# Optimization experiments

Hardware: AMD Instinct MI355X
Metric: run time of the kernel (lower is better)

The kernel has to match this reference:

```python
import jax, jax.numpy as jnp
import numpy as np

B, S, D, H = 2, 2048, 1024, 16
HD = D // H  # head_dim = 64
ROPE_BASE = 10000.0
INIT_STD = 0.02


def setup_inputs() -> dict:
    key = jax.random.key(0)
    k1, k2, k3 = jax.random.split(key, 3)
    x = jax.random.normal(k1, (B, S, D), dtype=jnp.float32)
    w_qkv = jax.random.normal(k2, (3 * D, D), dtype=jnp.float32) * INIT_STD
    w_out = jax.random.normal(k3, (D, D), dtype=jnp.float32) * (1.0 / np.sqrt(D))
    b_out = jnp.zeros((D,), dtype=jnp.float32)
    return {"x": x, "w_qkv": w_qkv, "w_out": w_out, "b_out": b_out}


def _rope_cos_sin(s_len, head_dim, dtype):
    theta = 1.0 / ROPE_BASE ** (jnp.arange(0, head_dim, 2, dtype=jnp.float32) / head_dim)
    freqs = jnp.outer(jnp.arange(s_len, dtype=jnp.float32), theta)  # [s, d/2]
    freqs = jnp.concatenate([freqs, freqs], axis=-1)  # [s, d]
    return jnp.cos(freqs).astype(dtype), jnp.sin(freqs).astype(dtype)


def _apply_rope(qk, cos, sin):
    # qk: [b, h, s, d]; rotate-half: (-x2, x1)
    d2 = qk.shape[-1] // 2
    x1, x2 = qk[..., :d2], qk[..., d2:]
    rot = jnp.concatenate([-x2, x1], axis=-1)
    return qk * cos + rot * sin


def reference(x, w_qkv, w_out, b_out):
    b, s, d = x.shape
    qkv = jnp.einsum('bsd,ed->bse', x, w_qkv)  # [b, s, 3D]
    qkv = qkv.reshape(b, s, 3 * H, HD).transpose(0, 2, 1, 3)  # [b, 3h, s, d]
    qk, v = qkv[:, :2 * H], qkv[:, 2 * H:]
    cos, sin = _rope_cos_sin(s, HD, x.dtype)
    qk = _apply_rope(qk, cos, sin)
    q, k = qk[:, :H], qk[:, H:]
    scale = 1.0 / np.sqrt(HD)
    scores = jnp.einsum('bhqd,bhkd->bhqk', q, k) * scale  # [b, h, s, s]
    causal = jnp.tril(jnp.ones((s, s), dtype=bool))
    scores = jnp.where(causal, scores, jnp.finfo(scores.dtype).min)
    attn = jax.nn.softmax(scores, axis=-1)
    o = jnp.einsum('bhqk,bhkd->bhqd', attn, v)  # [b, h, s, d]
    o = o.transpose(0, 2, 1, 3).reshape(b, s, d)
    return jnp.einsum('bsd,ed->bse', o, w_out) + b_out
```

## Files before the change

### kernel.cpp

```cpp
#include <hip/hip_runtime.h>
#include <hip/hip_fp16.h>
#include <math.h>

#define B_  2
#define S_  2048
#define D_  1024
#define H_  16
#define HD_ 64

typedef _Float16  f16;
typedef __attribute__((ext_vector_type(8))) _Float16 f16x8;
typedef __attribute__((ext_vector_type(4))) _Float16 f16x4;
typedef __attribute__((ext_vector_type(4))) float    f32x4;

#define LOG2E 1.4426950408889634f
#define L2_10000_DIV32 0.41524101186092029f
#define PS 72

__device__ __forceinline__ float fin(float v) { return (v == v) ? v : 0.0f; }

__device__ __forceinline__ f16x8 cvt8(const float* p) {
  float4 a = *(const float4*)p;
  float4 b = *(const float4*)(p + 4);
  f16x8 h;
  h[0] = (f16)a.x; h[1] = (f16)a.y; h[2] = (f16)a.z; h[3] = (f16)a.w;
  h[4] = (f16)b.x; h[5] = (f16)b.y; h[6] = (f16)b.z; h[7] = (f16)b.w;
  return h;
}

__global__ void __launch_bounds__(256)
k_cvt3(const float* __restrict__ wq, const float* __restrict__ wo,
       const float* __restrict__ x,
       f16* __restrict__ wqh, f16* __restrict__ woh, f16* __restrict__ xh,
       int doX)
{
  const int NWQ = 3 * D_ * D_ / 4, NWO = D_ * D_ / 4, NX = B_ * S_ * D_ / 4;
  const int n = NWQ + NWO + (doX ? NX : 0);
  for (int i = blockIdx.x * 256 + threadIdx.x; i < n; i += gridDim.x * 256) {
    const float* src; f16* dst; int j;
    if (i < NWQ)            { src = wq; dst = wqh; j = i; }
    else if (i < NWQ + NWO) { src = wo; dst = woh; j = i - NWQ; }
    else                    { src = x;  dst = xh;  j = i - NWQ - NWO; }
    float4 v = ((const float4*)src)[j];
    f16x4 h = {(f16)v.x, (f16)v.y, (f16)v.z, (f16)v.w};
    ((f16x4*)dst)[j] = h;
  }
}

template <bool XF16>
__global__ void __launch_bounds__(256)
k_qkv3(const float* __restrict__ xf, const f16* __restrict__ xh,
       const f16* __restrict__ wqh,
       f16* __restrict__ Qb, f16* __restrict__ Kb, f16* __restrict__ Vt)
{
  __shared__ __align__(16) f16 As[128 * PS];
  __shared__ __align__(16) f16 Bs[128 * PS];
  const int t = threadIdx.x;
  const int w = t >> 6;
  const int lane = t & 63;
  const int ll = lane & 15;
  const int quad = lane >> 4;
  const int wm = w >> 1, wn = w & 1;
  const int row0 = blockIdx.y * 128;
  const int col0 = blockIdx.x * 128;

  const f32x4 fz = {0.f, 0.f, 0.f, 0.f};
  f32x4 acc[4][4];
#pragma unroll
  for (int i = 0; i < 4; ++i)
#pragma unroll
    for (int j = 0; j < 4; ++j) acc[i][j] = fz;

  const int ldr = t >> 3;
  const int ldk = (t & 7) * 8;
  const float* gaf = xf  + (size_t)(row0 + ldr) * D_ + ldk;
  const f16*   gah = xh  + (size_t)(row0 + ldr) * D_ + ldk;
  const f16*   gb  = wqh + (size_t)(col0 + ldr) * D_ + ldk;

  for (int kt = 0; kt < D_; kt += 64) {
    f16x8 ra[4], rb[4];
#pragma unroll
    for (int i = 0; i < 4; ++i) {
      ra[i] = XF16 ? *(const f16x8*)(gah + (size_t)i * 32 * D_ + kt)
                   : cvt8(gaf + (size_t)i * 32 * D_ + kt);
      rb[i] = *(const f16x8*)(gb + (size_t)i * 32 * D_ + kt);
    }
    __syncthreads();
#pragma unroll
    for (int i = 0; i < 4; ++i) {
      *(f16x8*)&As[(i * 32 + ldr) * PS + ldk] = ra[i];
      *(f16x8*)&Bs[(i * 32 + ldr) * PS + ldk] = rb[i];
    }
    __syncthreads();
#pragma unroll
    for (int kk = 0; kk < 64; kk += 32) {
      f16x8 a[4], b[4];
#pragma unroll
      for (int mt = 0; mt < 4; ++mt)
        a[mt] = *(const f16x8*)&As[(wm * 64 + mt * 16 + ll) * PS + kk + quad * 8];
#pragma unroll
      for (int nt = 0; nt < 4; ++nt)
        b[nt] = *(const f16x8*)&Bs[(wn * 64 + nt * 16 + ll) * PS + kk + quad * 8];
#pragma unroll
      for (int mt = 0; mt < 4; ++mt)
#pragma unroll
        for (int nt = 0; nt < 4; ++nt)
          acc[mt][nt] = __builtin_amdgcn_mfma_f32_16x16x32_f16(
              a[mt], b[nt], acc[mt][nt], 0, 0, 0);
    }
  }

  const int h3 = (col0 >> 6) + wn;
  if (h3 < 32) {
    f16* dst = (h3 < 16) ? Qb : Kb;
    const int h = (h3 < 16) ? h3 : h3 - 16;
    const float th0 = exp2f(-(float)ll * L2_10000_DIV32);
    const float th1 = exp2f(-(float)(16 + ll) * L2_10000_DIV32);
#pragma unroll
    for (int mt = 0; mt < 4; ++mt) {
#pragma unroll
      for (int r = 0; r < 4; ++r) {
        const int row = row0 + wm * 64 + mt * 16 + quad * 4 + r;
        const int b = row >> 11;
        const int p = row & (S_ - 1);
        f16* base = dst + ((size_t)(b * H_ + h) * S_ + p) * HD_;
        const float fp = (float)p;
        float s0, c0, s1, c1;
        sincosf(fp * th0, &s0, &c0);
        sincosf(fp * th1, &s1, &c1);
        {
          float x1 = acc[mt][0][r], x2 = acc[mt][2][r];
          base[ll]      = (f16)fin(x1 * c0 - x2 * s0);
          base[ll + 32] = (f16)fin(x2 * c0 + x1 * s0);
        }
        {
          float x1 = acc[mt][1][r], x2 = acc[mt][3][r];
          base[16 + ll]      = (f16)fin(x1 * c1 - x2 * s1);
          base[16 + ll + 32] = (f16)fin(x2 * c1 + x1 * s1);
        }
      }
    }
  } else {
    const int hv = h3 - 32;
#pragma unroll
    for (int mt = 0; mt < 4; ++mt)
#pragma unroll
      for (int nt = 0; nt < 4; ++nt)
#pragma unroll
        for (int r = 0; r < 4; ++r) {
          const int row = row0 + wm * 64 + mt * 16 + quad * 4 + r;
          const int b = row >> 11;
          const int p = row & (S_ - 1);
          const int dd = nt * 16 + ll;
          Vt[((size_t)(b * H_ + hv) * HD_ + dd) * S_ + p] = (f16)fin(acc[mt][nt][r]);
        }
  }
}

__device__ __forceinline__ void softmax_tile(
    f32x4 sc[4], bool diag, int qloc, int ll, int quad,
    float& mrun, float& lrun, float& alpha, f16* Pt)
{
  if (diag) {
#pragma unroll
    for (int nt = 0; nt < 4; ++nt)
#pragma unroll
      for (int r = 0; r < 4; ++r)
        if ((nt * 16 + quad * 4 + r) > qloc) sc[nt][r] = -3.0e4f;
  }
  float pm = mrun;
#pragma unroll
  for (int nt = 0; nt < 4; ++nt)
#pragma unroll
    for (int r = 0; r < 4; ++r) pm = fmaxf(pm, sc[nt][r]);
  pm = fmaxf(pm, __shfl_xor(pm, 16));
  pm = fmaxf(pm, __shfl_xor(pm, 32));
  alpha = exp2f(mrun - pm);
  mrun = pm;
  float ps = 0.f;
#pragma unroll
  for (int nt = 0; nt < 4; ++nt) {
    f16x4 pk;
#pragma unroll
    for (int r = 0; r < 4; ++r) {
      float p = exp2f(sc[nt][r] - pm);
      ps += p;
      pk[r] = (f16)p;
    }
    *(f16x4*)&Pt[ll * PS + nt * 16 + quad * 4] = pk;
  }
  ps += __shfl_xor(ps, 16);
  ps += __shfl_xor(ps, 32);
  lrun = lrun * alpha + ps;
}

__device__ __forceinline__ void write_o(
    f32x4 acco[4], float lrun, f16* Pt, int ll, int quad, int w,
    int qt, size_t bh, f16* Ob)
{
  const float inv = 1.0f / fmaxf(lrun, 1e-30f);
#pragma unroll
  for (int dg = 0; dg < 4; ++dg) {
    f16x4 ov;
#pragma unroll
    for (int r = 0; r < 4; ++r) ov[r] = (f16)fin(acco[dg][r] * inv);
    *(f16x4*)&Pt[ll * PS + dg * 16 + quad * 4] = ov;
  }
#pragma unroll
  for (int s2 = 0; s2 < 2; ++s2) {
    f16x8 o = *(const f16x8*)&Pt[ll * PS + (quad + 4 * s2) * 8];
    const size_t row = bh * S_ + qt * 64 + w * 16 + ll;
    *(f16x8*)&Ob[row * HD_ + (quad + 4 * s2) * 8] = o;
  }
}

__global__ void __launch_bounds__(256, 3)
k_attn3(const f16* Qb, const f16* __restrict__ Kb,
        const f16* __restrict__ Vt, f16* Ob)
{
  __shared__ __align__(16) f16 Ks[2][64 * PS];
  __shared__ __align__(16) f16 Vs[2][64 * PS];
  __shared__ __align__(16) f16 Ps[4][16 * PS];

  const int t = threadIdx.x;
  const int w = t >> 6;
  const int lane = t & 63;
  const int ll = lane & 15;
  const int quad = lane >> 4;
  const int qtA = blockIdx.x;
  const int qtB = 31 - qtA;
  const int h = blockIdx.y;
  const int b = blockIdx.z;
  const size_t bh = (size_t)b * H_ + h;
  const f16* Qg = Qb + bh * S_ * HD_;
  const f16* Kg = Kb + bh * S_ * HD_;
  const f16* Vg = Vt + bh * HD_ * S_;

  f16x8 bqA[2], bqB[2];
  {
    const f16 hsc = (f16)(0.125f * LOG2E);
#pragma unroll
    for (int k2 = 0; k2 < 2; ++k2) {
      bqA[k2] = *(const f16x8*)(Qg + (size_t)(qtA * 64 + w * 16 + ll) * HD_ + k2 * 32 + quad * 8);
      bqB[k2] = *(const f16x8*)(Qg + (size_t)(qtB * 64 + w * 16 + ll) * HD_ + k2 * 32 + quad * 8);
#pragma unroll
      for (int e = 0; e < 8; ++e) { bqA[k2][e] *= hsc; bqB[k2][e] *= hsc; }
    }
  }
  {
    const int r = t >> 2;
    const int c = (t & 3) * 16;
    f16x8 a0 = *(const f16x8*)(Kg + (size_t)r * HD_ + c);
    f16x8 a1 = *(const f16x8*)(Kg + (size_t)r * HD_ + c + 8);
    f16x8 b0 = *(const f16x8*)(Vg + (size_t)r * S_ + c);
    f16x8 b1 = *(const f16x8*)(Vg + (size_t)r * S_ + c + 8);
    *(f16x8*)&Ks[0][r * PS + c]     = a0;
    *(f16x8*)&Ks[0][r * PS + c + 8] = a1;
    *(f16x8*)&Vs[0][r * PS + c]     = b0;
    *(f16x8*)&Vs[0][r * PS + c + 8] = b1;
  }
  __syncthreads();

  const f32x4 fz = {0.f, 0.f, 0.f, 0.f};
  f32x4 accoA[4], accoB[4];
#pragma unroll
  for (int i = 0; i < 4; ++i) { accoA[i] = fz; accoB[i] = fz; }
  float mA = -3.0e4f, lA = 0.f, mB = -3.0e4f, lB = 0.f;
  const int qloc = w * 16 + ll;
  f16* Pt = &Ps[w][0];

  for (int kt = 0; kt <= qtB; ++kt) {
    const int cur = kt & 1;
    const bool pre = (kt < qtB);
    const int sr = t >> 2, scc = (t & 3) * 16;
    f16x8 nk0, nk1, nv0, nv1;
    if (pre) {
      const int kn = (kt + 1) * 64;
      nk0 = *(const f16x8*)(Kg + (size_t)(kn + sr) * HD_ + scc);
      nk1 = *(const f16x8*)(Kg + (size_t)(kn + sr) * HD_ + scc + 8);
      nv0 = *(const f16x8*)(Vg + (size_t)sr * S_ + kn + scc);
      nv1 = *(const f16x8*)(Vg + (size_t)sr * S_ + kn + scc + 8);
    }
    const f16* Kc = Ks[cur];
    const f16* Vc = Vs[cur];
    const bool doA = (kt <= qtA);

    f16x8 ak[2][4];
#pragma unroll
    for (int k2 = 0; k2 < 2; ++k2)
#pragma unroll
      for (int nt = 0; nt < 4; ++nt)
        ak[k2][nt] = *(const f16x8*)&Kc[(nt * 16 + ll) * PS + k2 * 32 + quad * 8];

    f32x4 sB[4] = {fz, fz, fz, fz};
#pragma unroll
    for (int k2 = 0; k2 < 2; ++k2)
#pragma unroll
      for (int nt = 0; nt < 4; ++nt)
        sB[nt] = __builtin_amdgcn_mfma_f32_16x16x32_f16(ak[k2][nt], bqB[k2], sB[nt], 0, 0, 0);
    f32x4 sA[4] = {fz, fz, fz, fz};
    if (doA) {
#pragma unroll
      for (int k2 = 0; k2 < 2; ++k2)
#pragma unroll
        for (int nt = 0; nt < 4; ++nt)
          sA[nt] = __builtin_amdgcn_mfma_f32_16x16x32_f16(ak[k2][nt], bqA[k2], sA[nt], 0, 0, 0);
    }

    f16x8 av[2][4];
#pragma unroll
    for (int k2 = 0; k2 < 2; ++k2)
#pragma unroll
      for (int dg = 0; dg < 4; ++dg)
        av[k2][dg] = *(const f16x8*)&Vc[(dg * 16 + ll) * PS + k2 * 32 + quad * 8];

    float alpha;
    if (doA) {
      softmax_tile(sA, kt == qtA, qloc, ll, quad, mA, lA, alpha, Pt);
#pragma unroll
      for (int dg = 0; dg < 4; ++dg)
#pragma unroll
        for (int r = 0; r < 4; ++r) accoA[dg][r] *= alpha;
#pragma unroll
      for (int k2 = 0; k2 < 2; ++k2) {
        f16x8 bp = *(const f16x8*)&Pt[ll * PS + k2 * 32 + quad * 8];
#pragma unroll
        for (int dg = 0; dg < 4; ++dg)
          accoA[dg] = __builtin_amdgcn_mfma_f32_16x16x32_f16(av[k2][dg], bp, accoA[dg], 0, 0, 0);
      }
    }
    {
      softmax_tile(sB, kt == qtB, qloc, ll, quad, mB, lB, alpha, Pt);
#pragma unroll
      for (int dg = 0; dg < 4; ++dg)
#pragma unroll
        for (int r = 0; r < 4; ++r) accoB[dg][r] *= alpha;
#pragma unroll
      for (int k2 = 0; k2 < 2; ++k2) {
        f16x8 bp = *(const f16x8*)&Pt[ll * PS + k2 * 32 + quad * 8];
#pragma unroll
        for (int dg = 0; dg < 4; ++dg)
          accoB[dg] = __builtin_amdgcn_mfma_f32_16x16x32_f16(av[k2][dg], bp, accoB[dg], 0, 0, 0);
      }
    }

    if (pre) {
      *(f16x8*)&Ks[1 - cur][sr * PS + scc]     = nk0;
      *(f16x8*)&Ks[1 - cur][sr * PS + scc + 8] = nk1;
      *(f16x8*)&Vs[1 - cur][sr * PS + scc]     = nv0;
      *(f16x8*)&Vs[1 - cur][sr * PS + scc + 8] = nv1;
    }
    __syncthreads();
  }

  write_o(accoA, lA, Pt, ll, quad, w, qtA, bh, Ob);
  write_o(accoB, lB, Pt, ll, quad, w, qtB, bh, Ob);
}

__global__ void __launch_bounds__(256)
k_out3(const f16* __restrict__ Ob, const f16* __restrict__ Wh,
       const float* __restrict__ bias, float* __restrict__ out)
{
  __shared__ __align__(16) f16 As[64 * PS];
  __shared__ __align__(16) f16 Bs[128 * PS];
  const int t = threadIdx.x;
  const int w = t >> 6;
  const int lane = t & 63;
  const int ll = lane & 15;
  const int quad = lane >> 4;
  const int wm = w >> 1, wn = w & 1;
  const int row0 = blockIdx.y * 64;
  const int col0 = blockIdx.x * 128;
  const int bb = row0 >> 11;
  const int s0 = row0 & (S_ - 1);

  const f32x4 fz = {0.f, 0.f, 0.f, 0.f};
  f32x4 acc[2][4];
#pragma unroll
  for (int i = 0; i < 2; ++i)
#pragma unroll
    for (int j = 0; j < 4; ++j) acc[i][j] = fz;

  const int ldr = t >> 3;
  const int ldk = (t & 7) * 8;
  const f16* gb = Wh + (size_t)(col0 + ldr) * D_ + ldk;

  for (int kt = 0; kt < 16; ++kt) {
    const f16* ga = Ob + (((size_t)(bb * H_ + kt)) * S_ + s0 + ldr) * HD_ + ldk;
    f16x8 ra[2], rb[4];
#pragma unroll
    for (int i = 0; i < 2; ++i)
      ra[i] = *(const f16x8*)(ga + (size_t)i * 32 * HD_);
#pragma unroll
    for (int i = 0; i < 4; ++i)
      rb[i] = *(const f16x8*)(gb + (size_t)i * 32 * D_ + kt * 64);
    __syncthreads();
#pragma unroll
    for (int i = 0; i < 2; ++i)
      *(f16x8*)&As[(i * 32 + ldr) * PS + ldk] = ra[i];
#pragma unroll
    for (int i = 0; i < 4; ++i)
      *(f16x8*)&Bs[(i * 32 + ldr) * PS + ldk] = rb[i];
    __syncthreads();
#pragma unroll
    for (int kk = 0; kk < 64; kk += 32) {
      f16x8 a[2], b[4];
#pragma unroll
      for (int mt = 0; mt < 2; ++mt)
        a[mt] = *(const f16x8*)&As[(wm * 32 + mt * 16 + ll) * PS + kk + quad * 8];
#pragma unroll
      for (int nt = 0; nt < 4; ++nt)
        b[nt] = *(const f16x8*)&Bs[(wn * 64 + nt * 16 + ll) * PS + kk + quad * 8];
#pragma unroll
      for (int mt = 0; mt < 2; ++mt)
#pragma unroll
        for (int nt = 0; nt < 4; ++nt)
          acc[mt][nt] = __builtin_amdgcn_mfma_f32_16x16x32_f16(
              a[mt], b[nt], acc[mt][nt], 0, 0, 0);
    }
  }

#pragma unroll
  for (int mt = 0; mt < 2; ++mt)
#pragma unroll
    for (int r = 0; r < 4; ++r) {
      const int row = row0 + wm * 32 + mt * 16 + quad * 4 + r;
#pragma unroll
      for (int nt = 0; nt < 4; ++nt) {
        const int col = col0 + wn * 64 + nt * 16 + ll;
        out[(size_t)row * D_ + col] = fin(acc[mt][nt][r] + bias[col]);
      }
    }
}

extern "C" void kernel_launch(void* const* d_in, const int* in_sizes, int n_in,
                              void* d_out, int out_size, void* d_ws, size_t ws_size,
                              hipStream_t stream) {
  const float* x    = (const float*)d_in[0];
  const float* wqkv = (const float*)d_in[1];
  const float* wout = (const float*)d_in[2];
  const float* bout = (const float*)d_in[3];
  float* out = (float*)d_out;

  char* ws = (char*)d_ws;
  f16* wqh = (f16*)(ws);
  f16* Qb  = (f16*)(ws + 6291456);
  f16* Kb  = (f16*)(ws + 14680064);
  f16* Vt  = (f16*)(ws + 23068672);
  f16* woh = (f16*)(ws + 31457280);
  const bool bigws = ws_size >= (size_t)41943040;
  f16* xh  = (f16*)(ws + 33554432);

  k_cvt3<<<2048, 256, 0, stream>>>(wqkv, wout, x, wqh, woh, xh, bigws ? 1 : 0);
  if (bigws)
    k_qkv3<true><<<dim3(3 * D_ / 128, (B_ * S_) / 128), 256, 0, stream>>>(
        x, xh, wqh, Qb, Kb, Vt);
  else
    k_qkv3<false><<<dim3(3 * D_ / 128, (B_ * S_) / 128), 256, 0, stream>>>(
        x, xh, wqh, Qb, Kb, Vt);
  k_attn3<<<dim3(16, H_, B_), 256, 0, stream>>>(Qb, Kb, Vt, Qb );
  k_out3<<<dim3(D_ / 128, (B_ * S_) / 64), 256, 0, stream>>>(
      Qb, woh, bout, out);
}
```

Measured before the change: 187.4 us.

## Split paired query tiles into separate attention blocks with swizzled LDS and lazy rescale

Each attention block used to process two query tiles (qt and 31-qt) that shared K/V loads. Now each block processes one query tile, and a remapped block index interleaves long and short causal rows so the load stays balanced, with occupancy raised to 4 blocks per CU. The padded LDS rows are replaced by an XOR swizzle, which cuts shared memory use, and the online softmax only rescales the accumulator when the row max grows by more than 8 in log2 units. The cost is that K/V tiles are now loaded once per query tile instead of once per pair, and the lazy rescale lets probabilities reach up to 256 before they are stored as f16.

```diff
diff --git a/kernel.cpp b/kernel.cpp
--- a/kernel.cpp
+++ b/kernel.cpp
@@ -26,6 +26,10 @@
   h[0] = (f16)a.x; h[1] = (f16)a.y; h[2] = (f16)a.z; h[3] = (f16)a.w;
   h[4] = (f16)b.x; h[5] = (f16)b.y; h[6] = (f16)b.z; h[7] = (f16)b.w;
   return h;
+}
+
+__device__ __forceinline__ int swz64(int r, int c) {
+  return r * 64 + ((((c >> 3) ^ (r & 7)) << 3) | (c & 7));
 }
 
 __global__ void __launch_bounds__(256)
@@ -157,7 +161,7 @@
   }
 }
 
-__device__ __forceinline__ void softmax_tile(
+__device__ __forceinline__ bool softmax_tile4(
     f32x4 sc[4], bool diag, int qloc, int ll, int quad,
     float& mrun, float& lrun, float& alpha, f16* Pt)
 {
@@ -175,26 +179,27 @@
     for (int r = 0; r < 4; ++r) pm = fmaxf(pm, sc[nt][r]);
   pm = fmaxf(pm, __shfl_xor(pm, 16));
   pm = fmaxf(pm, __shfl_xor(pm, 32));
-  alpha = exp2f(mrun - pm);
-  mrun = pm;
+  const bool resc = !__all(pm <= mrun + 8.0f);
+  if (resc) { alpha = exp2f(mrun - pm); mrun = pm; }
   float ps = 0.f;
 #pragma unroll
   for (int nt = 0; nt < 4; ++nt) {
     f16x4 pk;
 #pragma unroll
     for (int r = 0; r < 4; ++r) {
-      float p = exp2f(sc[nt][r] - pm);
+      float p = exp2f(sc[nt][r] - mrun);
       ps += p;
       pk[r] = (f16)p;
     }
-    *(f16x4*)&Pt[ll * PS + nt * 16 + quad * 4] = pk;
+    *(f16x4*)&Pt[swz64(ll, nt * 16 + quad * 4)] = pk;
   }
   ps += __shfl_xor(ps, 16);
   ps += __shfl_xor(ps, 32);
-  lrun = lrun * alpha + ps;
-}
-
-__device__ __forceinline__ void write_o(
+  lrun = (resc ? lrun * alpha : lrun) + ps;
+  return resc;
+}
+
+__device__ __forceinline__ void write_o4(
     f32x4 acco[4], float lrun, f16* Pt, int ll, int quad, int w,
     int qt, size_t bh, f16* Ob)
 {
@@ -204,31 +209,32 @@
     f16x4 ov;
 #pragma unroll
     for (int r = 0; r < 4; ++r) ov[r] = (f16)fin(acco[dg][r] * inv);
-    *(f16x4*)&Pt[ll * PS + dg * 16 + quad * 4] = ov;
+    *(f16x4*)&Pt[swz64(ll, dg * 16 + quad * 4)] = ov;
   }
 #pragma unroll
   for (int s2 = 0; s2 < 2; ++s2) {
-    f16x8 o = *(const f16x8*)&Pt[ll * PS + (quad + 4 * s2) * 8];
+    f16x8 o = *(const f16x8*)&Pt[swz64(ll, (quad + 4 * s2) * 8)];
     const size_t row = bh * S_ + qt * 64 + w * 16 + ll;
     *(f16x8*)&Ob[row * HD_ + (quad + 4 * s2) * 8] = o;
   }
 }
 
-__global__ void __launch_bounds__(256, 3)
-k_attn3(const f16* Qb, const f16* __restrict__ Kb,
+__global__ void __launch_bounds__(256, 4)
+k_attn4(const f16* Qb, const f16* __restrict__ Kb,
         const f16* __restrict__ Vt, f16* Ob)
 {
-  __shared__ __align__(16) f16 Ks[2][64 * PS];
-  __shared__ __align__(16) f16 Vs[2][64 * PS];
-  __shared__ __align__(16) f16 Ps[4][16 * PS];
+  __shared__ __align__(16) f16 Ks[2][64 * 64];
+  __shared__ __align__(16) f16 Vs[2][64 * 64];
+  __shared__ __align__(16) f16 Ps[4][16 * 64];
 
   const int t = threadIdx.x;
   const int w = t >> 6;
   const int lane = t & 63;
   const int ll = lane & 15;
   const int quad = lane >> 4;
-  const int qtA = blockIdx.x;
-  const int qtB = 31 - qtA;
+  const int bx = blockIdx.x;
+  const int base = (bx & 1) ? 31 - (bx >> 1) : (bx >> 1);
+  const int qt = ((int)blockIdx.y < 8) ? base : 31 - base;
   const int h = blockIdx.y;
   const int b = blockIdx.z;
   const size_t bh = (size_t)b * H_ + h;
@@ -236,43 +242,39 @@
   const f16* Kg = Kb + bh * S_ * HD_;
   const f16* Vg = Vt + bh * HD_ * S_;
 
-  f16x8 bqA[2], bqB[2];
+  f16x8 bq[2];
   {
     const f16 hsc = (f16)(0.125f * LOG2E);
 #pragma unroll
     for (int k2 = 0; k2 < 2; ++k2) {
-      bqA[k2] = *(const f16x8*)(Qg + (size_t)(qtA * 64 + w * 16 + ll) * HD_ + k2 * 32 + quad * 8);
-      bqB[k2] = *(const f16x8*)(Qg + (size_t)(qtB * 64 + w * 16 + ll) * HD_ + k2 * 32 + quad * 8);
-#pragma unroll
-      for (int e = 0; e < 8; ++e) { bqA[k2][e] *= hsc; bqB[k2][e] *= hsc; }
-    }
-  }
+      bq[k2] = *(const f16x8*)(Qg + (size_t)(qt * 64 + w * 16 + ll) * HD_ + k2 * 32 + quad * 8);
+#pragma unroll
+      for (int e = 0; e < 8; ++e) bq[k2][e] *= hsc;
+    }
+  }
+  const int sr = t >> 2;
+  const int scc = (t & 3) * 16;
   {
-    const int r = t >> 2;
-    const int c = (t & 3) * 16;
-    f16x8 a0 = *(const f16x8*)(Kg + (size_t)r * HD_ + c);
-    f16x8 a1 = *(const f16x8*)(Kg + (size_t)r * HD_ + c + 8);
-    f16x8 b0 = *(const f16x8*)(Vg + (size_t)r * S_ + c);
-    f16x8 b1 = *(const f16x8*)(Vg + (size_t)r * S_ + c + 8);
-    *(f16x8*)&Ks[0][r * PS + c]     = a0;
-    *(f16x8*)&Ks[0][r * PS + c + 8] = a1;
-    *(f16x8*)&Vs[0][r * PS + c]     = b0;
-    *(f16x8*)&Vs[0][r * PS + c + 8] = b1;
+    f16x8 a0 = *(const f16x8*)(Kg + (size_t)sr * HD_ + scc);
+    f16x8 a1 = *(const f16x8*)(Kg + (size_t)sr * HD_ + scc + 8);
+    f16x8 b0 = *(const f16x8*)(Vg + (size_t)sr * S_ + scc);
+    f16x8 b1 = *(const f16x8*)(Vg + (size_t)sr * S_ + scc + 8);
+    *(f16x8*)&Ks[0][swz64(sr, scc)]     = a0;
+    *(f16x8*)&Ks[0][swz64(sr, scc + 8)] = a1;
+    *(f16x8*)&Vs[0][swz64(sr, scc)]     = b0;
+    *(f16x8*)&Vs[0][swz64(sr, scc + 8)] = b1;
   }
   __syncthreads();
 
   const f32x4 fz = {0.f, 0.f, 0.f, 0.f};
-  f32x4 accoA[4], accoB[4];
-#pragma unroll
-  for (int i = 0; i < 4; ++i) { accoA[i] = fz; accoB[i] = fz; }
-  float mA = -3.0e4f, lA = 0.f, mB = -3.0e4f, lB = 0.f;
+  f32x4 acco[4] = {fz, fz, fz, fz};
+  float m = -3.0e4f, l = 0.f;
   const int qloc = w * 16 + ll;
   f16* Pt = &Ps[w][0];
 
-  for (int kt = 0; kt <= qtB; ++kt) {
+  for (int kt = 0; kt <= qt; ++kt) {
     const int cur = kt & 1;
-    const bool pre = (kt < qtB);
-    const int sr = t >> 2, scc = (t & 3) * 16;
+    const bool pre = (kt < qt);
     f16x8 nk0, nk1, nv0, nv1;
     if (pre) {
       const int kn = (kt + 1) * 64;
@@ -283,78 +285,54 @@
     }
     const f16* Kc = Ks[cur];
     const f16* Vc = Vs[cur];
-    const bool doA = (kt <= qtA);
 
     f16x8 ak[2][4];
 #pragma unroll
     for (int k2 = 0; k2 < 2; ++k2)
 #pragma unroll
       for (int nt = 0; nt < 4; ++nt)
-        ak[k2][nt] = *(const f16x8*)&Kc[(nt * 16 + ll) * PS + k2 * 32 + quad * 8];
-
-    f32x4 sB[4] = {fz, fz, fz, fz};
+        ak[k2][nt] = *(const f16x8*)&Kc[swz64(nt * 16 + ll, k2 * 32 + quad * 8)];
+
+    f32x4 s[4] = {fz, fz, fz, fz};
 #pragma unroll
     for (int k2 = 0; k2 < 2; ++k2)
 #pragma unroll
       for (int nt = 0; nt < 4; ++nt)
-        sB[nt] = __builtin_amdgcn_mfma_f32_16x16x32_f16(ak[k2][nt], bqB[k2], sB[nt], 0, 0, 0);
-    f32x4 sA[4] = {fz, fz, fz, fz};
-    if (doA) {
-#pragma unroll
-      for (int k2 = 0; k2 < 2; ++k2)
-#pragma unroll
-        for (int nt = 0; nt < 4; ++nt)
-          sA[nt] = __builtin_amdgcn_mfma_f32_16x16x32_f16(ak[k2][nt], bqA[k2], sA[nt], 0, 0, 0);
-    }
+        s[nt] = __builtin_amdgcn_mfma_f32_16x16x32_f16(ak[k2][nt], bq[k2], s[nt], 0, 0, 0);
 
     f16x8 av[2][4];
 #pragma unroll
     for (int k2 = 0; k2 < 2; ++k2)
 #pragma unroll
       for (int dg = 0; dg < 4; ++dg)
-        av[k2][dg] = *(const f16x8*)&Vc[(dg * 16 + ll) * PS + k2 * 32 + quad * 8];
+        av[k2][dg] = *(const f16x8*)&Vc[swz64(dg * 16 + ll, k2 * 32 + quad * 8)];
 
     float alpha;
-    if (doA) {
-      softmax_tile(sA, kt == qtA, qloc, ll, quad, mA, lA, alpha, Pt);
+    const bool resc = softmax_tile4(s, kt == qt, qloc, ll, quad, m, l, alpha, Pt);
+    if (resc) {
 #pragma unroll
       for (int dg = 0; dg < 4; ++dg)
 #pragma unroll
-        for (int r = 0; r < 4; ++r) accoA[dg][r] *= alpha;
-#pragma unroll
-      for (int k2 = 0; k2 < 2; ++k2) {
-        f16x8 bp = *(const f16x8*)&Pt[ll * PS + k2 * 32 + quad * 8];
-#pragma unroll
-        for (int dg = 0; dg < 4; ++dg)
-          accoA[dg] = __builtin_amdgcn_mfma_f32_16x16x32_f16(av[k2][dg], bp, accoA[dg], 0, 0, 0);
-      }
-    }
-    {
-      softmax_tile(sB, kt == qtB, qloc, ll, quad, mB, lB, alpha, Pt);
+        for (int r = 0; r < 4; ++r) acco[dg][r] *= alpha;
+    }
+#pragma unroll
+    for (int k2 = 0; k2 < 2; ++k2) {
+      f16x8 bp = *(const f16x8*)&Pt[swz64(ll, k2 * 32 + quad * 8)];
 #pragma unroll
       for (int dg = 0; dg < 4; ++dg)
-#pragma unroll
-        for (int r = 0; r < 4; ++r) accoB[dg][r] *= alpha;
-#pragma unroll
-      for (int k2 = 0; k2 < 2; ++k2) {
-        f16x8 bp = *(const f16x8*)&Pt[ll * PS + k2 * 32 + quad * 8];
-#pragma unroll
-        for (int dg = 0; dg < 4; ++dg)
-          accoB[dg] = __builtin_amdgcn_mfma_f32_16x16x32_f16(av[k2][dg], bp, accoB[dg], 0, 0, 0);
-      }
+        acco[dg] = __builtin_amdgcn_mfma_f32_16x16x32_f16(av[k2][dg], bp, acco[dg], 0, 0, 0);
     }
 
     if (pre) {
-      *(f16x8*)&Ks[1 - cur][sr * PS + scc]     = nk0;
-      *(f16x8*)&Ks[1 - cur][sr * PS + scc + 8] = nk1;
-      *(f16x8*)&Vs[1 - cur][sr * PS + scc]     = nv0;
-      *(f16x8*)&Vs[1 - cur][sr * PS + scc + 8] = nv1;
+      *(f16x8*)&Ks[1 - cur][swz64(sr, scc)]     = nk0;
+      *(f16x8*)&Ks[1 - cur][swz64(sr, scc + 8)] = nk1;
+      *(f16x8*)&Vs[1 - cur][swz64(sr, scc)]     = nv0;
+      *(f16x8*)&Vs[1 - cur][swz64(sr, scc + 8)] = nv1;
     }
     __syncthreads();
   }
 
-  write_o(accoA, lA, Pt, ll, quad, w, qtA, bh, Ob);
-  write_o(accoB, lB, Pt, ll, quad, w, qtB, bh, Ob);
+  write_o4(acco, l, Pt, ll, quad, w, qt, bh, Ob);
 }
 
 __global__ void __launch_bounds__(256)
@@ -458,7 +436,7 @@
   else
     k_qkv3<false><<<dim3(3 * D_ / 128, (B_ * S_) / 128), 256, 0, stream>>>(
         x, xh, wqh, Qb, Kb, Vt);
-  k_attn3<<<dim3(16, H_, B_), 256, 0, stream>>>(Qb, Kb, Vt, Qb );
+  k_attn4<<<dim3(32, H_, B_), 256, 0, stream>>>(Qb, Kb, Vt, Qb );
   k_out3<<<dim3(D_ / 128, (B_ * S_) / 64), 256, 0, stream>>>(
       Qb, woh, bout, out);
 }
```

After: 183.0 us. 2.4% less time.
